# Kernel tuning notes

Measured on AMD Instinct MI355X. Metric: run time of the kernel, lower is better.

Reference implementation:

```python
import jax, jax.numpy as jnp
import numpy as np

B, K, H = 8, 64, 2048
NH, NKV, HD = 16, 4, 128
CTX = 4096
EPS = 1e-6


def _rope_tables(batch, total_len, head_dim):
    inv_freq = 1.0 / (10000.0 ** (np.arange(0, head_dim, 2, dtype=np.float32) / head_dim))
    pos = np.arange(total_len, dtype=np.float32)
    freqs = np.outer(pos, inv_freq)                      # [S, D/2]
    emb = np.concatenate([freqs, freqs], axis=-1)        # [S, D]
    cos = np.broadcast_to(np.cos(emb), (batch, total_len, head_dim))
    sin = np.broadcast_to(np.sin(emb), (batch, total_len, head_dim))
    return jnp.asarray(cos), jnp.asarray(sin)


def setup_inputs() -> dict:
    key = jax.random.key(0)
    ks = jax.random.split(key, 10)
    s = 0.02
    cos, sin = _rope_tables(B, CTX + K, HD)
    return {
        "hidden_states": jax.random.normal(ks[0], (B, K, H), jnp.float32),
        "ctx_k": jax.random.normal(ks[1], (B, CTX, NKV, HD), jnp.float32),
        "ctx_v": jax.random.normal(ks[2], (B, CTX, NKV, HD), jnp.float32),
        "attn_mask": jnp.zeros((B, 1, K, CTX + K), jnp.float32),
        "cos": cos,
        "sin": sin,
        "wq": jax.random.normal(ks[3], (NH * HD, H), jnp.float32) * s,
        "wk": jax.random.normal(ks[4], (NKV * HD, H), jnp.float32) * s,
        "wv": jax.random.normal(ks[5], (NKV * HD, H), jnp.float32) * s,
        "wo": jax.random.normal(ks[6], (H, NH * HD), jnp.float32) * s,
        "q_norm_w": jnp.ones((HD,), jnp.float32),
        "k_norm_w": jnp.ones((HD,), jnp.float32),
    }


def _rms_norm(x, w):
    var = jnp.mean(jnp.square(x), axis=-1, keepdims=True)
    return x * jax.lax.rsqrt(var + EPS) * w


def _rotate_half(x):
    x1, x2 = jnp.split(x, 2, axis=-1)
    return jnp.concatenate([-x2, x1], axis=-1)


def reference(hidden_states, ctx_k, ctx_v, attn_mask, cos, sin,
              wq, wk, wv, wo, q_norm_w, k_norm_w):
    b, k_len, _ = hidden_states.shape
    ctx_len = ctx_k.shape[1]
    groups = NH // NKV

    # projections -> [B, heads, S, D]
    q = (hidden_states @ wq.T).reshape(b, k_len, NH, HD).transpose(0, 2, 1, 3)
    k_noise = (hidden_states @ wk.T).reshape(b, k_len, NKV, HD).transpose(0, 2, 1, 3)
    v_noise = (hidden_states @ wv.T).reshape(b, k_len, NKV, HD).transpose(0, 2, 1, 3)

    # concat context KV (already per-head projected) with noise KV
    k = jnp.concatenate([ctx_k.transpose(0, 2, 1, 3), k_noise], axis=2)  # [B,NKV,ctx+K,D]
    v = jnp.concatenate([ctx_v.transpose(0, 2, 1, 3), v_noise], axis=2)

    # QK RMSNorm over head_dim
    q = _rms_norm(q, q_norm_w)
    k = _rms_norm(k, k_norm_w)

    # RoPE: q occupies the last K positions, k spans all ctx+K positions
    cos_q = cos[:, ctx_len:, :][:, None, :, :]
    sin_q = sin[:, ctx_len:, :][:, None, :, :]
    cos_k = cos[:, None, :, :]
    sin_k = sin[:, None, :, :]
    q = q * cos_q + _rotate_half(q) * sin_q
    k = k * cos_k + _rotate_half(k) * sin_k

    # GQA expand kv heads -> NH heads
    k = jnp.repeat(k, groups, axis=1)  # [B,NH,ctx+K,D]
    v = jnp.repeat(v, groups, axis=1)

    # scaled dot product attention with float mask
    scale = 1.0 / jnp.sqrt(jnp.float32(HD))
    scores = jnp.einsum("bhqd,bhkd->bhqk", q, k) * scale + attn_mask
    probs = jax.nn.softmax(scores, axis=-1)
    attn = jnp.einsum("bhqk,bhkd->bhqd", probs, v)

    out = attn.transpose(0, 2, 1, 3).reshape(b, k_len, NH * HD)
    return out @ wo.T
```

## Files before the change

### kernel.cpp

```cpp
#include <hip/hip_runtime.h>

#define BB   8
#define KQ   64
#define HDIM 2048
#define NH   16
#define NKV  4
#define HD   128
#define CTX  4096
#define TTOT 4160
#define NTILES 65
#define LOG2E 1.4426950408889634f
#define SCALE 0.08838834764831845f
#define QSCALE (SCALE * LOG2E)
#define MFIX 16.34f

typedef unsigned short u16;
typedef unsigned int   u32;
typedef __attribute__((ext_vector_type(8))) short  s16x8;
typedef __attribute__((ext_vector_type(4))) unsigned short u16x4;
typedef __attribute__((ext_vector_type(4))) float  f32x4;
typedef __bf16 bf16x8 __attribute__((ext_vector_type(8)));

__device__ __forceinline__ u16 f2bf(float f) {
    union { __bf16 h; u16 u; } v; v.h = (__bf16)f; return v.u;
}
__device__ __forceinline__ float bf2f(u16 u) {
    union { float f; u32 u; } v; v.u = ((u32)u) << 16;
    return v.f;
}
__device__ __forceinline__ u32 pack2(float a, float b) {
    return (u32)f2bf(a) | ((u32)f2bf(b) << 16);
}
__device__ __forceinline__ f32x4 mfma16(bf16x8 a, bf16x8 b, f32x4 c) {
    return __builtin_amdgcn_mfma_f32_16x16x32_bf16(a, b, c, 0, 0, 0);
}

__global__ __launch_bounds__(256) void cast_all(
    const float* __restrict__ wq, const float* __restrict__ wk,
    const float* __restrict__ wv, const float* __restrict__ wo,
    const float* __restrict__ hs,
    u16* __restrict__ wqkvb, u16* __restrict__ wob, u16* __restrict__ hsb)
{
    const int i = blockIdx.x * 256 + threadIdx.x;
    const float* src; u16* dst;
    if (i < 524288)       { src = wq + (size_t)i * 8;             dst = wqkvb + (size_t)i * 8; }
    else if (i < 655360)  { src = wk + (size_t)(i - 524288) * 8;  dst = wqkvb + (size_t)i * 8; }
    else if (i < 786432)  { src = wv + (size_t)(i - 655360) * 8;  dst = wqkvb + (size_t)i * 8; }
    else if (i < 1310720) { src = wo + (size_t)(i - 786432) * 8;  dst = wob + (size_t)(i - 786432) * 8; }
    else                  { src = hs + (size_t)(i - 1310720) * 8; dst = hsb + (size_t)(i - 1310720) * 8; }
    float4 a = *(const float4*)src;
    float4 b = *(const float4*)(src + 4);
    s16x8 v;
    v[0]=(short)f2bf(a.x); v[1]=(short)f2bf(a.y); v[2]=(short)f2bf(a.z); v[3]=(short)f2bf(a.w);
    v[4]=(short)f2bf(b.x); v[5]=(short)f2bf(b.y); v[6]=(short)f2bf(b.z); v[7]=(short)f2bf(b.w);
    *(s16x8*)dst = v;
}

__device__ __forceinline__ void gemm64_body(
    const u16* __restrict__ Ab, const u16* __restrict__ Bb,
    float* __restrict__ Cb, const int ldc, const int ldk, const int Klen,
    u16* Ash, u16* Bsh)
{
    const int tid = threadIdx.x, lane = tid & 63;
    const int w = tid >> 6, wm = w >> 1, wn = w & 1;
    const int l15 = lane & 15, l4 = lane >> 4;
    const int srow = tid >> 2, scol = (tid & 3) * 16;

    f32x4 acc[2][2];
#pragma unroll
    for (int i = 0; i < 2; ++i)
#pragma unroll
        for (int j = 0; j < 2; ++j) acc[i][j] = (f32x4){0.f, 0.f, 0.f, 0.f};

    const u16* ap = Ab + (size_t)srow * ldk + scol;
    const u16* bp = Bb + (size_t)srow * ldk + scol;
    s16x8 ra0 = *(const s16x8*)ap, ra1 = *(const s16x8*)(ap + 8);
    s16x8 rb0 = *(const s16x8*)bp, rb1 = *(const s16x8*)(bp + 8);
    __builtin_amdgcn_sched_barrier(0);

    for (int k0 = 0; k0 < Klen; k0 += 64) {
        __syncthreads();
        *(s16x8*)(Ash + srow * 72 + scol)     = ra0;
        *(s16x8*)(Ash + srow * 72 + scol + 8) = ra1;
        *(s16x8*)(Bsh + srow * 72 + scol)     = rb0;
        *(s16x8*)(Bsh + srow * 72 + scol + 8) = rb1;
        __syncthreads();
        if (k0 + 64 < Klen) {
            const u16* ap2 = ap + k0 + 64;
            const u16* bp2 = bp + k0 + 64;
            ra0 = *(const s16x8*)ap2; ra1 = *(const s16x8*)(ap2 + 8);
            rb0 = *(const s16x8*)bp2; rb1 = *(const s16x8*)(bp2 + 8);
            __builtin_amdgcn_sched_barrier(0);
        }
#pragma unroll
        for (int ks = 0; ks < 2; ++ks) {
            bf16x8 am[2], bb[2];
#pragma unroll
            for (int i = 0; i < 2; ++i) {
                am[i] = *(const bf16x8*)(Ash + (wm * 32 + i * 16 + l15) * 72 + ks * 32 + l4 * 8);
                bb[i] = *(const bf16x8*)(Bsh + (wn * 32 + i * 16 + l15) * 72 + ks * 32 + l4 * 8);
            }
#pragma unroll
            for (int i = 0; i < 2; ++i)
#pragma unroll
                for (int j = 0; j < 2; ++j)
                    acc[i][j] = mfma16(am[i], bb[j], acc[i][j]);
        }
    }

    float* Cw = Cb + (size_t)(wm * 32) * ldc + wn * 32;
#pragma unroll
    for (int i = 0; i < 2; ++i)
#pragma unroll
        for (int j = 0; j < 2; ++j)
#pragma unroll
            for (int r = 0; r < 4; ++r)
                Cw[(size_t)(i * 16 + l4 * 4 + r) * ldc + j * 16 + l15] = acc[i][j][r];
}

__global__ __launch_bounds__(256) void gemm_qkv_sk(
    const u16* __restrict__ hsb, const u16* __restrict__ wqkvb,
    float* __restrict__ qkvp)
{
    __shared__ __align__(16) u16 Ash[64 * 72];
    __shared__ __align__(16) u16 Bsh[64 * 72];
    const int wid = (blockIdx.x & 7) * 192 + (blockIdx.x >> 3);
    const int y = wid >> 5, rem = wid & 31, kc = rem >> 3, x = rem & 7;
    const int koff = kc * 512;
    const u16* Ab = hsb + (size_t)x * 64 * HDIM + koff;
    const u16* Bb = wqkvb + (size_t)y * 64 * HDIM + koff;
    float* Cb = qkvp + (size_t)kc * 512 * 3072 + (size_t)x * 64 * 3072 + y * 64;
    gemm64_body(Ab, Bb, Cb, 3072, HDIM, 512, Ash, Bsh);
}

__global__ __launch_bounds__(256) void gemm_out_sk(
    const u16* __restrict__ attnb, const u16* __restrict__ wob,
    float* __restrict__ outp)
{
    __shared__ __align__(16) u16 Ash[64 * 72];
    __shared__ __align__(16) u16 Bsh[64 * 72];
    const int wid = (blockIdx.x & 7) * 128 + (blockIdx.x >> 3);
    const int y = wid >> 5, rem = wid & 31, kc = rem >> 3, x = rem & 7;
    const int koff = kc * 512;
    const u16* Ab = attnb + (size_t)x * 64 * HDIM + koff;
    const u16* Bb = wob + (size_t)y * 64 * HDIM + koff;
    float* Cb = outp + (size_t)kc * 512 * 2048 + (size_t)x * 64 * 2048 + y * 64;
    gemm64_body(Ab, Bb, Cb, 2048, HDIM, 512, Ash, Bsh);
}

__global__ __launch_bounds__(256) void reduce4(
    const float* __restrict__ p, float* __restrict__ out, const size_t chunk)
{
    const size_t i = ((size_t)blockIdx.x * 256 + threadIdx.x) * 4;
    float4 a = *(const float4*)(p + i);
    float4 b = *(const float4*)(p + i + chunk);
    float4 c = *(const float4*)(p + i + 2 * chunk);
    float4 d = *(const float4*)(p + i + 3 * chunk);
    float4 r;
    r.x = (a.x + b.x) + (c.x + d.x);
    r.y = (a.y + b.y) + (c.y + d.y);
    r.z = (a.z + b.z) + (c.z + d.z);
    r.w = (a.w + b.w) + (c.w + d.w);
    *(float4*)(out + i) = r;
}

__device__ __forceinline__ void norm_rope_vals(
    float2 xa, float2 xb, const float* __restrict__ wgt,
    const float* __restrict__ cosT, const float* __restrict__ sinT,
    int pos, int j, float outScale, u16* __restrict__ dst)
{
    float ss = xa.x * xa.x + xa.y * xa.y + xb.x * xb.x + xb.y * xb.y;
#pragma unroll
    for (int m = 1; m < 32; m <<= 1) ss += __shfl_xor(ss, m);
    const float rr = rsqrtf(ss * (1.0f / 128.0f) + 1e-6f);
    float2 wa = *(const float2*)(wgt + 2 * j);
    float2 wb = *(const float2*)(wgt + 2 * j + 64);
    float2 ca = *(const float2*)(cosT + (size_t)pos * 128 + 2 * j);
    float2 sa = *(const float2*)(sinT + (size_t)pos * 128 + 2 * j);
    const float nax = xa.x * rr * wa.x, nay = xa.y * rr * wa.y;
    const float nbx = xb.x * rr * wb.x, nby = xb.y * rr * wb.y;
    const float lox = (nax * ca.x - nbx * sa.x) * outScale;
    const float loy = (nay * ca.y - nby * sa.y) * outScale;
    const float hix = (nbx * ca.x + nax * sa.x) * outScale;
    const float hiy = (nby * ca.y + nay * sa.y) * outScale;
    ((u32*)dst)[j]      = pack2(lox, loy);
    ((u32*)dst)[j + 32] = pack2(hix, hiy);
}

__global__ __launch_bounds__(256) void finalize_qkv(
    const float* __restrict__ qkvp, const float* __restrict__ qw,
    const float* __restrict__ kw, const float* __restrict__ cosT,
    const float* __restrict__ sinT,
    u16* __restrict__ Qb, u16* __restrict__ knb, u16* __restrict__ vnb)
{
    const int unit = blockIdx.x * 8 + (threadIdx.x >> 5);
    const int j = threadIdx.x & 31;
    const int slot = unit % 24, bq = unit / 24;
    const int b = bq >> 6, q = bq & 63;
    const int col0 = (slot < 16) ? slot * 128
                   : (slot < 20) ? 2048 + (slot - 16) * 128
                                 : 2560 + (slot - 20) * 128;
    const float* base = qkvp + (size_t)bq * 3072 + col0;

    float2 xa = {0.f, 0.f}, xb = {0.f, 0.f};
#pragma unroll
    for (int kc = 0; kc < 4; ++kc) {
        const float* p = base + (size_t)kc * 512 * 3072;
        float2 a = *(const float2*)(p + 2 * j);
        float2 c = *(const float2*)(p + 2 * j + 64);
        xa.x += a.x; xa.y += a.y; xb.x += c.x; xb.y += c.y;
    }

    if (slot < 16) {
        norm_rope_vals(xa, xb, qw, cosT, sinT, CTX + q, j, QSCALE,
                       Qb + ((size_t)((b * 16 + slot) * 64 + q)) * 128);
    } else if (slot < 20) {
        norm_rope_vals(xa, xb, kw, cosT, sinT, CTX + q, j, 1.0f,
                       knb + ((size_t)((b * 4 + (slot - 16)) * 64 + q)) * 128);
    } else {
        u16* dst = vnb + ((size_t)((b * 4 + (slot - 20)) * 64 + q)) * 128;
        ((u32*)dst)[j]      = pack2(xa.x, xa.y);
        ((u32*)dst)[j + 32] = pack2(xb.x, xb.y);
    }
}

__global__ __launch_bounds__(256) void build_ctx_k(
    const float* __restrict__ ctxk, const float* __restrict__ kw,
    const float* __restrict__ cosT, const float* __restrict__ sinT,
    const u16* __restrict__ knb, u16* __restrict__ Kb)
{
    const int bid = blockIdx.x;
    if (bid < 4096) {
        const int unit = bid * 8 + (threadIdx.x >> 5);
        const int j = threadIdx.x & 31;
        const int b = unit >> 12, pos = unit & 4095;
        float2 ca = *(const float2*)(cosT + (size_t)pos * 128 + 2 * j);
        float2 sa = *(const float2*)(sinT + (size_t)pos * 128 + 2 * j);
        float2 wa = *(const float2*)(kw + 2 * j);
        float2 wb = *(const float2*)(kw + 2 * j + 64);
        const float* src0 = ctxk + (size_t)unit * 512;
        float2 xa[4], xb[4];
#pragma unroll
        for (int kv = 0; kv < 4; ++kv) {
            xa[kv] = *(const float2*)(src0 + kv * 128 + 2 * j);
            xb[kv] = *(const float2*)(src0 + kv * 128 + 2 * j + 64);
        }
        float ss[4];
#pragma unroll
        for (int kv = 0; kv < 4; ++kv)
            ss[kv] = xa[kv].x * xa[kv].x + xa[kv].y * xa[kv].y
                   + xb[kv].x * xb[kv].x + xb[kv].y * xb[kv].y;
#pragma unroll
        for (int m = 1; m < 32; m <<= 1) {
#pragma unroll
            for (int kv = 0; kv < 4; ++kv) ss[kv] += __shfl_xor(ss[kv], m);
        }
#pragma unroll
        for (int kv = 0; kv < 4; ++kv) {
            const float rr = rsqrtf(ss[kv] * (1.0f / 128.0f) + 1e-6f);
            const float nax = xa[kv].x * rr * wa.x, nay = xa[kv].y * rr * wa.y;
            const float nbx = xb[kv].x * rr * wb.x, nby = xb[kv].y * rr * wb.y;
            u16* dst = Kb + ((size_t)(b * 4 + kv) * TTOT + pos) * 128;
            ((u32*)dst)[j]      = pack2(nax * ca.x - nbx * sa.x, nay * ca.y - nby * sa.y);
            ((u32*)dst)[j + 32] = pack2(nbx * ca.x + nax * sa.x, nby * ca.y + nay * sa.y);
        }
    } else {
        const int idx = bid - 4096;
        const u16* src = knb + (size_t)idx * 64 * 128;
        u16* dst = Kb + ((size_t)idx * TTOT + 4096) * 128;
#pragma unroll
        for (int it = 0; it < 4; ++it) {
            const int e = (it * 256 + threadIdx.x) * 8;
            *(s16x8*)(dst + e) = *(const s16x8*)(src + e);
        }
    }
}

__global__ __launch_bounds__(256) void build_ctx_v(
    const float* __restrict__ ctxv, const u16* __restrict__ vnb,
    u16* __restrict__ VtG)
{
    __shared__ __align__(16) float Vt[64 * 130];
    const int bid = blockIdx.x;
    if (bid < 2048) {
        const int pt = bid & 63, kv = (bid >> 6) & 3, b = bid >> 8;
        const int p0 = pt * 64;
        const float* src = ctxv + ((size_t)(b * 4096 + p0) * 4 + kv) * 128;
#pragma unroll
        for (int it = 0; it < 8; ++it) {
            const int g = it * 256 + threadIdx.x;
            const int row = g >> 5, c4 = (g & 31) * 4;
            *(float4*)(&Vt[row * 130 + c4]) = *(const float4*)(src + (size_t)row * 512 + c4);
        }
        __syncthreads();
        const int d = threadIdx.x & 127, half = threadIdx.x >> 7;
        u16* dst = VtG + ((size_t)(b * 4 + kv) * 128 + d) * TTOT + p0 + half * 32;
#pragma unroll
        for (int q8 = 0; q8 < 4; ++q8) {
            s16x8 v;
#pragma unroll
            for (int je = 0; je < 8; ++je)
                v[je] = (short)f2bf(Vt[(half * 32 + q8 * 8 + je) * 130 + d]);
            *(s16x8*)(dst + q8 * 8) = v;
        }
    } else {
        const int idx = bid - 2048;
        const u16* src = vnb + (size_t)idx * 64 * 128;
        u16* dstb = VtG + (size_t)idx * 128 * TTOT + 4096;
        const int d = threadIdx.x & 127, qh = threadIdx.x >> 7;
        u16* dst = dstb + (size_t)d * TTOT + qh * 32;
#pragma unroll
        for (int q8 = 0; q8 < 4; ++q8) {
            s16x8 v;
#pragma unroll
            for (int je = 0; je < 8; ++je)
                v[je] = (short)src[(size_t)(qh * 32 + q8 * 8 + je) * 128 + d];
            *(s16x8*)(dst + q8 * 8) = v;
        }
    }
}

template <int S>
__global__ __launch_bounds__(512, 2) void attn_partial(
    const u16* __restrict__ Qb, const u16* __restrict__ Kb, const u16* __restrict__ VtG,
    const float* __restrict__ mask, u16* __restrict__ Opart, float* __restrict__ lsum)
{
    __shared__ __align__(16) u16   Ksh[2][64 * 136];
    __shared__ __align__(16) u16   Vsh[2][128 * 72];
    __shared__ __align__(16) float Msh[2][64 * 68];
    __shared__ __align__(16) u16   Psh[8][32 * 40];

    const int s = blockIdx.x, kv = blockIdx.y, b = blockIdx.z;
    const int tid = threadIdx.x, lane = tid & 63, w = tid >> 6;
    const int h = kv * 4 + (w >> 1);
    const int qh = w & 1, qbase = qh * 32;
    const int l15 = lane & 15, l4 = lane >> 4;
    const int t0 = (NTILES * s) / S, t1 = (NTILES * (s + 1)) / S;

    bf16x8 aq[2][4];
    {
        const u16* qb = Qb + ((size_t)((b * 16 + h) * 64 + qbase)) * 128;
#pragma unroll
        for (int mt = 0; mt < 2; ++mt)
#pragma unroll
            for (int ks = 0; ks < 4; ++ks)
                aq[mt][ks] = *(const bf16x8*)(qb + (mt * 16 + l15) * 128 + ks * 32 + l4 * 8);
    }

    bf16x8 bones;
    {
        __bf16 e = (l15 == 0) ? (__bf16)1.0f : (__bf16)0.0f;
#pragma unroll
        for (int i = 0; i < 8; ++i) bones[i] = e;
    }

    f32x4 o[2][8], ol[2];
#pragma unroll
    for (int mt = 0; mt < 2; ++mt) {
        ol[mt] = (f32x4){0.f, 0.f, 0.f, 0.f};
#pragma unroll
        for (int nt = 0; nt < 8; ++nt) o[mt][nt] = (f32x4){0.f, 0.f, 0.f, 0.f};
    }

    const u16* Kbase = Kb + (size_t)(b * 4 + kv) * TTOT * 128;
    const u16* Vbase = VtG + (size_t)(b * 4 + kv) * 128 * TTOT;
    const float* mrow = mask + (size_t)b * 64 * TTOT;
    u16* P = Psh[w];

    const int kp = tid >> 4, kd8 = (tid & 15) * 8;
    const int vr = tid >> 3, vc8 = (tid & 7) * 8;
    const int mq_ = tid >> 3, mk8 = (tid & 7) * 8;

    s16x8 rk0, rk1, rv0, rv1;
    float4 rm0, rm1;

    auto ld = [&](int t) {
        const int p = t * 64;
        rk0 = *(const s16x8*)(Kbase + (size_t)(p + kp) * 128 + kd8);
        rk1 = *(const s16x8*)(Kbase + (size_t)(p + kp + 32) * 128 + kd8);
        rv0 = *(const s16x8*)(Vbase + (size_t)vr * TTOT + p + vc8);
        rv1 = *(const s16x8*)(Vbase + (size_t)(vr + 64) * TTOT + p + vc8);
        const float* mp = mrow + (size_t)mq_ * TTOT + p + mk8;
        rm0 = *(const float4*)mp;
        rm1 = *(const float4*)(mp + 4);
        __builtin_amdgcn_sched_barrier(0);
    };
    auto st = [&](int buf) {
        *(s16x8*)(Ksh[buf] + kp * 136 + kd8) = rk0;
        *(s16x8*)(Ksh[buf] + (kp + 32) * 136 + kd8) = rk1;
        *(s16x8*)(Vsh[buf] + vr * 72 + vc8) = rv0;
        *(s16x8*)(Vsh[buf] + (vr + 64) * 72 + vc8) = rv1;
        float* md = Msh[buf] + mq_ * 68 + mk8;
        md[0] = fmaf(rm0.x, LOG2E, -MFIX); md[1] = fmaf(rm0.y, LOG2E, -MFIX);
        md[2] = fmaf(rm0.z, LOG2E, -MFIX); md[3] = fmaf(rm0.w, LOG2E, -MFIX);
        md[4] = fmaf(rm1.x, LOG2E, -MFIX); md[5] = fmaf(rm1.y, LOG2E, -MFIX);
        md[6] = fmaf(rm1.z, LOG2E, -MFIX); md[7] = fmaf(rm1.w, LOG2E, -MFIX);
    };

    ld(t0);
    st(0);
    __syncthreads();
    if (t0 + 1 < t1) ld(t0 + 1);

    int cur = 0;
    for (int t = t0; t < t1; ++t) {
        f32x4 sc[2][4];
#pragma unroll
        for (int mt = 0; mt < 2; ++mt)
#pragma unroll
            for (int nt = 0; nt < 4; ++nt) sc[mt][nt] = (f32x4){0.f, 0.f, 0.f, 0.f};
        __builtin_amdgcn_s_setprio(1);
#pragma unroll
        for (int nt = 0; nt < 4; ++nt) {
#pragma unroll
            for (int ks = 0; ks < 4; ++ks) {
                bf16x8 bk = *(const bf16x8*)(Ksh[cur] + (nt * 16 + l15) * 136 + ks * 32 + l4 * 8);
                sc[0][nt] = mfma16(aq[0][ks], bk, sc[0][nt]);
                sc[1][nt] = mfma16(aq[1][ks], bk, sc[1][nt]);
            }
        }
        __builtin_amdgcn_s_setprio(0);

#pragma unroll
        for (int mt = 0; mt < 2; ++mt) {
#pragma unroll
            for (int r = 0; r < 4; ++r) {
                const int q = qbase + mt * 16 + l4 * 4 + r;
                const float* mq = Msh[cur] + q * 68 + l15;
                sc[mt][0][r] = exp2f(sc[mt][0][r] + mq[0]);
                sc[mt][1][r] = exp2f(sc[mt][1][r] + mq[16]);
                sc[mt][2][r] = exp2f(sc[mt][2][r] + mq[32]);
                sc[mt][3][r] = exp2f(sc[mt][3][r] + mq[48]);
            }
        }

#pragma unroll
        for (int ks = 0; ks < 2; ++ks) {
#pragma unroll
            for (int mt = 0; mt < 2; ++mt)
#pragma unroll
                for (int r = 0; r < 4; ++r) {
                    P[(mt * 16 + l4 * 4 + r) * 40 + l15]      = f2bf(sc[mt][ks * 2 + 0][r]);
                    P[(mt * 16 + l4 * 4 + r) * 40 + 16 + l15] = f2bf(sc[mt][ks * 2 + 1][r]);
                }
            bf16x8 ap0 = *(const bf16x8*)(P + (l15) * 40 + l4 * 8);
            bf16x8 ap1 = *(const bf16x8*)(P + (16 + l15) * 40 + l4 * 8);
            __builtin_amdgcn_s_setprio(1);
#pragma unroll
            for (int nt = 0; nt < 8; ++nt) {
                bf16x8 bv = *(const bf16x8*)(Vsh[cur] + (nt * 16 + l15) * 72 + ks * 32 + l4 * 8);
                o[0][nt] = mfma16(ap0, bv, o[0][nt]);
                o[1][nt] = mfma16(ap1, bv, o[1][nt]);
            }
            ol[0] = mfma16(ap0, bones, ol[0]);
            ol[1] = mfma16(ap1, bones, ol[1]);
            __builtin_amdgcn_s_setprio(0);
        }

        if (t + 1 < t1) st(cur ^ 1);
        __syncthreads();
        if (t + 2 < t1) ld(t + 2);
        cur ^= 1;
    }

    {
        u16* ob = Opart + ((size_t)((b * 16 + h) * S + s)) * 8192;
#pragma unroll
        for (int mt = 0; mt < 2; ++mt)
#pragma unroll
            for (int nt = 0; nt < 8; ++nt) {
                u16x4 v;
#pragma unroll
                for (int r = 0; r < 4; ++r) v[r] = f2bf(o[mt][nt][r]);
                *(u16x4*)(ob + (((qh * 2 + mt) * 8 + nt) * 64 + lane) * 4) = v;
            }
        if (l15 == 0) {
#pragma unroll
            for (int mt = 0; mt < 2; ++mt)
#pragma unroll
                for (int r = 0; r < 4; ++r) {
                    const int q = qbase + mt * 16 + l4 * 4 + r;
                    lsum[((size_t)((b * 16 + h) * 64 + q)) * S + s] = ol[mt][r];
                }
        }
    }
}

template <int S>
__global__ __launch_bounds__(256) void merge_kernel(
    const u16* __restrict__ Opart, const float* __restrict__ lsum, u16* __restrict__ attnb)
{
    const int wid = blockIdx.x * 4 + (threadIdx.x >> 6);
    const int lane = threadIdx.x & 63;
    const int l15 = lane & 15, l4 = lane >> 4;
    const int qh = wid & 1, bh = wid >> 1;
    const int h = bh & 15, b = bh >> 4;

    float L = 0.f;
    {
        const float* lr = lsum + ((size_t)bh * 64 + qh * 32 + (lane & 31)) * S;
#pragma unroll
        for (int s2 = 0; s2 < S; ++s2) L += lr[s2];
    }
    const float invL = 1.0f / L;

    float acc[2][8][4];
#pragma unroll
    for (int mt = 0; mt < 2; ++mt)
#pragma unroll
        for (int nt = 0; nt < 8; ++nt)
#pragma unroll
            for (int r = 0; r < 4; ++r) acc[mt][nt][r] = 0.f;

    for (int s2 = 0; s2 < S; ++s2) {
        const u16* ob = Opart + ((size_t)(bh * S + s2)) * 8192;
#pragma unroll
        for (int mt = 0; mt < 2; ++mt)
#pragma unroll
            for (int nt = 0; nt < 8; ++nt) {
                u16x4 v = *(const u16x4*)(ob + (((qh * 2 + mt) * 8 + nt) * 64 + lane) * 4);
#pragma unroll
                for (int r = 0; r < 4; ++r) acc[mt][nt][r] += bf2f(v[r]);
            }
    }

#pragma unroll
    for (int mt = 0; mt < 2; ++mt)
#pragma unroll
        for (int r = 0; r < 4; ++r) {
            const float wl = __shfl(invL, mt * 16 + l4 * 4 + r);
            const int q = qh * 32 + mt * 16 + l4 * 4 + r;
            u16* dst = attnb + (size_t)(b * 64 + q) * 2048 + h * 128;
#pragma unroll
            for (int nt = 0; nt < 8; ++nt)
                dst[nt * 16 + l15] = f2bf(acc[mt][nt][r] * wl);
        }
}

extern "C" void kernel_launch(void* const* d_in, const int* in_sizes, int n_in,
                              void* d_out, int out_size, void* d_ws, size_t ws_size,
                              hipStream_t stream)
{
    (void)in_sizes; (void)n_in; (void)out_size; (void)ws_size;
    const float* hs   = (const float*)d_in[0];
    const float* ctxk = (const float*)d_in[1];
    const float* ctxv = (const float*)d_in[2];
    const float* mask = (const float*)d_in[3];
    const float* cosT = (const float*)d_in[4];
    const float* sinT = (const float*)d_in[5];
    const float* wq   = (const float*)d_in[6];
    const float* wk   = (const float*)d_in[7];
    const float* wv   = (const float*)d_in[8];
    const float* wo   = (const float*)d_in[9];
    const float* qnw  = (const float*)d_in[10];
    const float* knw  = (const float*)d_in[11];

    const int S = 8;

    char* ws = (char*)d_ws;
    size_t off = 0;
    auto carve = [&](size_t bytes) -> void* {
        void* p = ws + off;
        off += (bytes + 255) & ~(size_t)255;
        return p;
    };
    u16*   Qb    = (u16*)carve((size_t)BB * NH * 64 * 128 * 2);
    u16*   Kb    = (u16*)carve((size_t)BB * NKV * TTOT * 128 * 2);
    u16*   VtG   = (u16*)carve((size_t)BB * NKV * TTOT * 128 * 2);
    u16*   Opart = (u16*)carve((size_t)BB * NH * S * 8192 * 2);
    float* lsumb = (float*)carve((size_t)BB * NH * 64 * S * 4);
    u16*   attnb = (u16*)carve((size_t)512 * 2048 * 2);
    u16*   wob   = (u16*)carve((size_t)2048 * 2048 * 2);
    u16*   knb   = (u16*)carve((size_t)BB * NKV * 64 * 128 * 2);
    u16*   vnb   = (u16*)carve((size_t)BB * NKV * 64 * 128 * 2);
    u16*   wqkvb = (u16*)Kb;
    float* qkvp  = (float*)VtG;
    u16*   hsb   = (u16*)Opart;
    float* outp  = (float*)Kb;

    cast_all<<<5632, 256, 0, stream>>>(wq, wk, wv, wo, hs, wqkvb, wob, hsb);
    gemm_qkv_sk<<<1536, 256, 0, stream>>>(hsb, wqkvb, qkvp);
    finalize_qkv<<<1536, 256, 0, stream>>>(qkvp, qnw, knw, cosT, sinT, Qb, knb, vnb);
    build_ctx_k<<<4128, 256, 0, stream>>>(ctxk, knw, cosT, sinT, knb, Kb);
    build_ctx_v<<<2080, 256, 0, stream>>>(ctxv, vnb, VtG);
    attn_partial<8><<<dim3(8, NKV, BB), 512, 0, stream>>>(Qb, Kb, VtG, mask, Opart, lsumb);
    merge_kernel<8><<<64, 256, 0, stream>>>(Opart, lsumb, attnb);
    gemm_out_sk<<<1024, 256, 0, stream>>>(attnb, wob, outp);
    reduce4<<<1024, 256, 0, stream>>>(outp, (float*)d_out, (size_t)512 * 2048);
}
```

Before: 138.2 us.

## Precompute transposed bf16 log2-scaled mask and vectorize ctx-K norm/RoPE

Adds a prep_mask kernel that converts the float mask to bf16, pre-applies the log2e scale and offset, and transposes it to position-major layout. The attention kernel then loads and stores a single 16-byte mask vector per tile and reads four values per lane in one LDS access, cutting mask bandwidth and per-tile arithmetic. build_ctx_k is reorganized so each wave handles one position with float4 loads and a shorter shuffle reduction. The cost is an extra kernel launch and extra global traffic for the mask copy, plus bf16 rounding of mask values, which is only exact for masks that bf16 represents well.

```diff
diff --git a/kernel.cpp b/kernel.cpp
--- a/kernel.cpp
+++ b/kernel.cpp
@@ -54,6 +54,39 @@
     v[0]=(short)f2bf(a.x); v[1]=(short)f2bf(a.y); v[2]=(short)f2bf(a.z); v[3]=(short)f2bf(a.w);
     v[4]=(short)f2bf(b.x); v[5]=(short)f2bf(b.y); v[6]=(short)f2bf(b.z); v[7]=(short)f2bf(b.w);
     *(s16x8*)dst = v;
+}
+
+__global__ __launch_bounds__(256) void prep_mask(
+    const float* __restrict__ mask, u16* __restrict__ maskT)
+{
+    __shared__ float T[64 * 65];
+    const int pt = blockIdx.x % 65, b = blockIdx.x / 65;
+    const int p0 = pt * 64;
+    {
+        const int q = threadIdx.x >> 2, pg = (threadIdx.x & 3) * 16;
+        const float* src = mask + ((size_t)b * 64 + q) * TTOT + p0 + pg;
+#pragma unroll
+        for (int v4 = 0; v4 < 4; ++v4) {
+            float4 v = *(const float4*)(src + v4 * 4);
+            T[q * 65 + pg + v4 * 4 + 0] = fmaf(v.x, LOG2E, -MFIX);
+            T[q * 65 + pg + v4 * 4 + 1] = fmaf(v.y, LOG2E, -MFIX);
+            T[q * 65 + pg + v4 * 4 + 2] = fmaf(v.z, LOG2E, -MFIX);
+            T[q * 65 + pg + v4 * 4 + 3] = fmaf(v.w, LOG2E, -MFIX);
+        }
+    }
+    __syncthreads();
+    {
+        const int pos = threadIdx.x >> 2, qg = (threadIdx.x & 3) * 16;
+        u16* dst = maskT + ((size_t)b * TTOT + p0 + pos) * 64 + qg;
+#pragma unroll
+        for (int h8 = 0; h8 < 2; ++h8) {
+            s16x8 v;
+#pragma unroll
+            for (int je = 0; je < 8; ++je)
+                v[je] = (short)f2bf(T[(qg + h8 * 8 + je) * 65 + pos]);
+            *(s16x8*)(dst + h8 * 8) = v;
+        }
+    }
 }
 
 __device__ __forceinline__ void gemm64_body(
@@ -230,42 +263,43 @@
     const u16* __restrict__ knb, u16* __restrict__ Kb)
 {
     const int bid = blockIdx.x;
-    if (bid < 4096) {
-        const int unit = bid * 8 + (threadIdx.x >> 5);
-        const int j = threadIdx.x & 31;
+    if (bid < 8192) {
+        const int unit = bid * 4 + (threadIdx.x >> 6);
+        const int lane = threadIdx.x & 63;
+        const int kv = lane >> 4, seg = lane & 15;
         const int b = unit >> 12, pos = unit & 4095;
-        float2 ca = *(const float2*)(cosT + (size_t)pos * 128 + 2 * j);
-        float2 sa = *(const float2*)(sinT + (size_t)pos * 128 + 2 * j);
-        float2 wa = *(const float2*)(kw + 2 * j);
-        float2 wb = *(const float2*)(kw + 2 * j + 64);
-        const float* src0 = ctxk + (size_t)unit * 512;
-        float2 xa[4], xb[4];
-#pragma unroll
-        for (int kv = 0; kv < 4; ++kv) {
-            xa[kv] = *(const float2*)(src0 + kv * 128 + 2 * j);
-            xb[kv] = *(const float2*)(src0 + kv * 128 + 2 * j + 64);
-        }
-        float ss[4];
-#pragma unroll
-        for (int kv = 0; kv < 4; ++kv)
-            ss[kv] = xa[kv].x * xa[kv].x + xa[kv].y * xa[kv].y
-                   + xb[kv].x * xb[kv].x + xb[kv].y * xb[kv].y;
-#pragma unroll
-        for (int m = 1; m < 32; m <<= 1) {
-#pragma unroll
-            for (int kv = 0; kv < 4; ++kv) ss[kv] += __shfl_xor(ss[kv], m);
-        }
-#pragma unroll
-        for (int kv = 0; kv < 4; ++kv) {
-            const float rr = rsqrtf(ss[kv] * (1.0f / 128.0f) + 1e-6f);
-            const float nax = xa[kv].x * rr * wa.x, nay = xa[kv].y * rr * wa.y;
-            const float nbx = xb[kv].x * rr * wb.x, nby = xb[kv].y * rr * wb.y;
-            u16* dst = Kb + ((size_t)(b * 4 + kv) * TTOT + pos) * 128;
-            ((u32*)dst)[j]      = pack2(nax * ca.x - nbx * sa.x, nay * ca.y - nby * sa.y);
-            ((u32*)dst)[j + 32] = pack2(nbx * ca.x + nax * sa.x, nby * ca.y + nay * sa.y);
-        }
+        const float* src = ctxk + ((size_t)unit * 4 + kv) * 128 + seg * 4;
+        float4 xa = *(const float4*)src;
+        float4 xb = *(const float4*)(src + 64);
+        float ss = xa.x * xa.x + xa.y * xa.y + xa.z * xa.z + xa.w * xa.w
+                 + xb.x * xb.x + xb.y * xb.y + xb.z * xb.z + xb.w * xb.w;
+        ss += __shfl_xor(ss, 1);
+        ss += __shfl_xor(ss, 2);
+        ss += __shfl_xor(ss, 4);
+        ss += __shfl_xor(ss, 8);
+        const float rr = rsqrtf(ss * (1.0f / 128.0f) + 1e-6f);
+        float4 ca = *(const float4*)(cosT + (size_t)pos * 128 + seg * 4);
+        float4 sa = *(const float4*)(sinT + (size_t)pos * 128 + seg * 4);
+        float4 wa = *(const float4*)(kw + seg * 4);
+        float4 wb = *(const float4*)(kw + 64 + seg * 4);
+        const float nax = xa.x * rr * wa.x, nay = xa.y * rr * wa.y;
+        const float naz = xa.z * rr * wa.z, naw = xa.w * rr * wa.w;
+        const float nbx = xb.x * rr * wb.x, nby = xb.y * rr * wb.y;
+        const float nbz = xb.z * rr * wb.z, nbw = xb.w * rr * wb.w;
+        u16x4 vlo, vhi;
+        vlo[0] = f2bf(nax * ca.x - nbx * sa.x);
+        vlo[1] = f2bf(nay * ca.y - nby * sa.y);
+        vlo[2] = f2bf(naz * ca.z - nbz * sa.z);
+        vlo[3] = f2bf(naw * ca.w - nbw * sa.w);
+        vhi[0] = f2bf(nbx * ca.x + nax * sa.x);
+        vhi[1] = f2bf(nby * ca.y + nay * sa.y);
+        vhi[2] = f2bf(nbz * ca.z + naz * sa.z);
+        vhi[3] = f2bf(nbw * ca.w + naw * sa.w);
+        u16* dst = Kb + ((size_t)(b * 4 + kv) * TTOT + pos) * 128 + seg * 4;
+        *(u16x4*)dst = vlo;
+        *(u16x4*)(dst + 64) = vhi;
     } else {
-        const int idx = bid - 4096;
+        const int idx = bid - 8192;
         const u16* src = knb + (size_t)idx * 64 * 128;
         u16* dst = Kb + ((size_t)idx * TTOT + 4096) * 128;
 #pragma unroll
@@ -323,12 +357,12 @@
 template <int S>
 __global__ __launch_bounds__(512, 2) void attn_partial(
     const u16* __restrict__ Qb, const u16* __restrict__ Kb, const u16* __restrict__ VtG,
-    const float* __restrict__ mask, u16* __restrict__ Opart, float* __restrict__ lsum)
-{
-    __shared__ __align__(16) u16   Ksh[2][64 * 136];
-    __shared__ __align__(16) u16   Vsh[2][128 * 72];
-    __shared__ __align__(16) float Msh[2][64 * 68];
-    __shared__ __align__(16) u16   Psh[8][32 * 40];
+    const u16* __restrict__ maskT, u16* __restrict__ Opart, float* __restrict__ lsum)
+{
+    __shared__ __align__(16) u16 Ksh[2][64 * 136];
+    __shared__ __align__(16) u16 Vsh[2][128 * 72];
+    __shared__ __align__(16) u16 Msh[2][64 * 72];
+    __shared__ __align__(16) u16 Psh[8][32 * 40];
 
     const int s = blockIdx.x, kv = blockIdx.y, b = blockIdx.z;
     const int tid = threadIdx.x, lane = tid & 63, w = tid >> 6;
@@ -364,15 +398,14 @@
 
     const u16* Kbase = Kb + (size_t)(b * 4 + kv) * TTOT * 128;
     const u16* Vbase = VtG + (size_t)(b * 4 + kv) * 128 * TTOT;
-    const float* mrow = mask + (size_t)b * 64 * TTOT;
+    const u16* mrow = maskT + (size_t)b * TTOT * 64;
     u16* P = Psh[w];
 
     const int kp = tid >> 4, kd8 = (tid & 15) * 8;
     const int vr = tid >> 3, vc8 = (tid & 7) * 8;
-    const int mq_ = tid >> 3, mk8 = (tid & 7) * 8;
-
-    s16x8 rk0, rk1, rv0, rv1;
-    float4 rm0, rm1;
+    const int mpos = tid >> 3, mq8 = (tid & 7) * 8;
+
+    s16x8 rk0, rk1, rv0, rv1, rm;
 
     auto ld = [&](int t) {
         const int p = t * 64;
@@ -380,9 +413,7 @@
         rk1 = *(const s16x8*)(Kbase + (size_t)(p + kp + 32) * 128 + kd8);
         rv0 = *(const s16x8*)(Vbase + (size_t)vr * TTOT + p + vc8);
         rv1 = *(const s16x8*)(Vbase + (size_t)(vr + 64) * TTOT + p + vc8);
-        const float* mp = mrow + (size_t)mq_ * TTOT + p + mk8;
-        rm0 = *(const float4*)mp;
-        rm1 = *(const float4*)(mp + 4);
+        rm  = *(const s16x8*)(mrow + (size_t)(p + mpos) * 64 + mq8);
         __builtin_amdgcn_sched_barrier(0);
     };
     auto st = [&](int buf) {
@@ -390,11 +421,7 @@
         *(s16x8*)(Ksh[buf] + (kp + 32) * 136 + kd8) = rk1;
         *(s16x8*)(Vsh[buf] + vr * 72 + vc8) = rv0;
         *(s16x8*)(Vsh[buf] + (vr + 64) * 72 + vc8) = rv1;
-        float* md = Msh[buf] + mq_ * 68 + mk8;
-        md[0] = fmaf(rm0.x, LOG2E, -MFIX); md[1] = fmaf(rm0.y, LOG2E, -MFIX);
-        md[2] = fmaf(rm0.z, LOG2E, -MFIX); md[3] = fmaf(rm0.w, LOG2E, -MFIX);
-        md[4] = fmaf(rm1.x, LOG2E, -MFIX); md[5] = fmaf(rm1.y, LOG2E, -MFIX);
-        md[6] = fmaf(rm1.z, LOG2E, -MFIX); md[7] = fmaf(rm1.w, LOG2E, -MFIX);
+        *(s16x8*)(Msh[buf] + mpos * 72 + mq8) = rm;
     };
 
     ld(t0);
@@ -424,13 +451,11 @@
 #pragma unroll
         for (int mt = 0; mt < 2; ++mt) {
 #pragma unroll
-            for (int r = 0; r < 4; ++r) {
-                const int q = qbase + mt * 16 + l4 * 4 + r;
-                const float* mq = Msh[cur] + q * 68 + l15;
-                sc[mt][0][r] = exp2f(sc[mt][0][r] + mq[0]);
-                sc[mt][1][r] = exp2f(sc[mt][1][r] + mq[16]);
-                sc[mt][2][r] = exp2f(sc[mt][2][r] + mq[32]);
-                sc[mt][3][r] = exp2f(sc[mt][3][r] + mq[48]);
+            for (int nt = 0; nt < 4; ++nt) {
+                u16x4 m4 = *(const u16x4*)(Msh[cur] + (nt * 16 + l15) * 72 + qbase + mt * 16 + l4 * 4);
+#pragma unroll
+                for (int r = 0; r < 4; ++r)
+                    sc[mt][nt][r] = exp2f(sc[mt][nt][r] + bf2f(m4[r]));
             }
         }
 
@@ -573,17 +598,19 @@
     u16*   wob   = (u16*)carve((size_t)2048 * 2048 * 2);
     u16*   knb   = (u16*)carve((size_t)BB * NKV * 64 * 128 * 2);
     u16*   vnb   = (u16*)carve((size_t)BB * NKV * 64 * 128 * 2);
+    u16*   maskT = (u16*)carve((size_t)BB * TTOT * 64 * 2);
     u16*   wqkvb = (u16*)Kb;
     float* qkvp  = (float*)VtG;
     u16*   hsb   = (u16*)Opart;
     float* outp  = (float*)Kb;
 
     cast_all<<<5632, 256, 0, stream>>>(wq, wk, wv, wo, hs, wqkvb, wob, hsb);
+    prep_mask<<<520, 256, 0, stream>>>(mask, maskT);
     gemm_qkv_sk<<<1536, 256, 0, stream>>>(hsb, wqkvb, qkvp);
     finalize_qkv<<<1536, 256, 0, stream>>>(qkvp, qnw, knw, cosT, sinT, Qb, knb, vnb);
-    build_ctx_k<<<4128, 256, 0, stream>>>(ctxk, knw, cosT, sinT, knb, Kb);
+    build_ctx_k<<<8224, 256, 0, stream>>>(ctxk, knw, cosT, sinT, knb, Kb);
     build_ctx_v<<<2080, 256, 0, stream>>>(ctxv, vnb, VtG);
-    attn_partial<8><<<dim3(8, NKV, BB), 512, 0, stream>>>(Qb, Kb, VtG, mask, Opart, lsumb);
+    attn_partial<8><<<dim3(8, NKV, BB), 512, 0, stream>>>(Qb, Kb, VtG, maskT, Opart, lsumb);
     merge_kernel<8><<<64, 256, 0, stream>>>(Opart, lsumb, attnb);
     gemm_out_sk<<<1024, 256, 0, stream>>>(attnb, wob, outp);
     reduce4<<<1024, 256, 0, stream>>>(outp, (float*)d_out, (size_t)512 * 2048);
```

After: 141.0 us. +2.1%, slower.
